# Kernel optimization log

Hardware: AMD Instinct MI355X
Metric: run time of the kernel (lower is better)

Reference implementation:

```python
import jax, jax.numpy as jnp
import numpy as np

CTX = 768   # ctx_len in the original module
C = 768     # n_embd
B = 16
T = 768
K_EPS = 1e-8


def setup_inputs() -> dict:
    key = jax.random.key(0)
    ks = jax.random.split(key, 10)
    scale = 1.0 / np.sqrt(C)
    x = jax.random.normal(ks[0], (B, T, C), jnp.float32)
    time_decay = jax.random.normal(ks[1], (C, 1), jnp.float32) * 0.1
    time_first = jnp.full((C, 1), np.log(0.3), jnp.float32)
    time_mix_k = jax.random.uniform(ks[2], (1, 1, C), jnp.float32)
    time_mix_v = jax.random.uniform(ks[3], (1, 1, C), jnp.float32)
    time_mix_r = jax.random.uniform(ks[4], (1, 1, C), jnp.float32)
    Wk = jax.random.normal(ks[5], (C, C), jnp.float32) * scale
    Wv = jax.random.normal(ks[6], (C, C), jnp.float32) * scale
    Wr = jax.random.normal(ks[7], (C, C), jnp.float32) * scale
    Wo = jax.random.normal(ks[8], (C, C), jnp.float32) * scale
    return {"x": x, "time_decay": time_decay, "time_first": time_first,
            "time_mix_k": time_mix_k, "time_mix_v": time_mix_v, "time_mix_r": time_mix_r,
            "Wk": Wk, "Wv": Wv, "Wr": Wr, "Wo": Wo}


def reference(x, time_decay, time_first, time_mix_k, time_mix_v, time_mix_r, Wk, Wv, Wr, Wo):
    Bb, Tt, Cc = x.shape
    # time_shift: xx[t] = x[t-1], xx[0] = 0
    xx = jnp.pad(x, ((0, 0), (1, 0), (0, 0)))[:, :Tt]
    xk = x * time_mix_k + xx * (1.0 - time_mix_k)
    xv = x * time_mix_v + xx * (1.0 - time_mix_v)
    xr = x * time_mix_r + xx * (1.0 - time_mix_r)
    # projections (nn.Linear, no bias: y = x @ W.T); k, v laid out [B, C, T]
    k = jnp.einsum('btc,oc->bot', xk, Wk)
    v = jnp.einsum('btc,oc->bot', xv, Wv)
    r = jnp.einsum('btc,oc->bto', xr, Wr)
    k = jnp.exp(jnp.minimum(k, 60.0))
    kv = k * v
    # decay kernel: time_w = cat([exp(time_decay)*time_curve, time_first]); w = exp(time_w)[:, -T:]
    curve = (jnp.arange(CTX - 1) - (CTX - 2)).astype(x.dtype)  # [-(CTX-2) .. 0]
    tw = jnp.concatenate([jnp.exp(time_decay) * curve[None, :], time_first], axis=-1)  # [C, CTX]
    w = jnp.exp(tw)[:, -Tt:]            # [C, T]
    kern = w[:, None, :]                # [C, 1, T] depthwise kernel

    def causal_conv(z):  # z: [B, C, T] -> [B, C, T], left-padded cross-correlation
        return jax.lax.conv_general_dilated(
            z, kern, window_strides=(1,), padding=[(Tt - 1, 0)],
            feature_group_count=Cc, dimension_numbers=('NCH', 'OIH', 'NCH'))

    wkv = causal_conv(kv)
    wk = causal_conv(k) + K_EPS
    rwkv = jax.nn.sigmoid(r) * jnp.transpose(wkv / wk, (0, 2, 1))  # [B, T, C]
    return jnp.einsum('btc,oc->bto', rwkv, Wo)
```

## Files before the change

kernel.cpp:

```cpp
#include <hip/hip_runtime.h>
#include <math.h>

#define Mq 12288
#define Nq 768
#define Kq 768
#define Tq 768
#define Bq 16
#define Cq 768
#define BK 64
#define BM 128

typedef __bf16 bf16x8 __attribute__((ext_vector_type(8)));
typedef __bf16 bf16x4 __attribute__((ext_vector_type(4)));
typedef __bf16 bf16x2 __attribute__((ext_vector_type(2)));
typedef float  floatx4 __attribute__((ext_vector_type(4)));

#define GLD_LDS16(g, l) __builtin_amdgcn_global_load_lds(                      \
    (const __attribute__((address_space(1))) unsigned int*)(g),                \
    (__attribute__((address_space(3))) unsigned int*)(l), 16, 0, 0)

__global__ __launch_bounds__(256)
void prep_kernel(const float* __restrict__ x,
                 const float* __restrict__ mk, const float* __restrict__ mv,
                 const float* __restrict__ mr,
                 const float* __restrict__ Wk, const float* __restrict__ Wv,
                 const float* __restrict__ Wr, const float* __restrict__ Wo,
                 __bf16* __restrict__ xk, __bf16* __restrict__ xv,
                 __bf16* __restrict__ xr, __bf16* __restrict__ wp)
{
    const int bid = blockIdx.x;
    if (bid < 9216) {
        const int i  = bid * 256 + threadIdx.x;
        const int c4 = i % (Cq / 4);
        const int m  = i / (Cq / 4);
        const int t  = m % Tq;
        const int c0 = c4 * 4;

        const float4 xc = *(const float4*)(x + (size_t)m * Cq + c0);
        float4 xp = make_float4(0.f, 0.f, 0.f, 0.f);
        if (t > 0) xp = *(const float4*)(x + (size_t)(m - 1) * Cq + c0);

        const float4 k4 = *(const float4*)(mk + c0);
        const float4 v4 = *(const float4*)(mv + c0);
        const float4 r4 = *(const float4*)(mr + c0);

        bf16x4 ok = { (__bf16)fmaf(k4.x, xc.x - xp.x, xp.x),
                      (__bf16)fmaf(k4.y, xc.y - xp.y, xp.y),
                      (__bf16)fmaf(k4.z, xc.z - xp.z, xp.z),
                      (__bf16)fmaf(k4.w, xc.w - xp.w, xp.w) };
        bf16x4 ov = { (__bf16)fmaf(v4.x, xc.x - xp.x, xp.x),
                      (__bf16)fmaf(v4.y, xc.y - xp.y, xp.y),
                      (__bf16)fmaf(v4.z, xc.z - xp.z, xp.z),
                      (__bf16)fmaf(v4.w, xc.w - xp.w, xp.w) };
        bf16x4 orr = { (__bf16)fmaf(r4.x, xc.x - xp.x, xp.x),
                       (__bf16)fmaf(r4.y, xc.y - xp.y, xp.y),
                       (__bf16)fmaf(r4.z, xc.z - xp.z, xp.z),
                       (__bf16)fmaf(r4.w, xc.w - xp.w, xp.w) };
        const size_t o = (size_t)m * Cq + c0;
        *(bf16x4*)(xk + o) = ok;
        *(bf16x4*)(xv + o) = ov;
        *(bf16x4*)(xr + o) = orr;
    } else {
        const int i   = (bid - 9216) * 256 + threadIdx.x;
        const int a   = i / 147456;
        const int off = (i - a * 147456) * 4;
        const float* s = (a == 0) ? Wk : (a == 1) ? Wv : (a == 2) ? Wr : Wo;
        const float4 v = *(const float4*)(s + off);
        bf16x4 r = { (__bf16)v.x, (__bf16)v.y, (__bf16)v.z, (__bf16)v.w };
        *(bf16x4*)(wp + (size_t)a * 589824 + off) = r;
    }
}

template<bool KVR>
__global__ __launch_bounds__(256, 3)
void mfma_gemm(const __bf16* __restrict__ A0, const __bf16* __restrict__ A1,
               const __bf16* __restrict__ A2,
               const __bf16* __restrict__ W,
               __bf16* __restrict__ OUTb, float* __restrict__ OUTf)
{
    __shared__ __bf16 As[BM * BK];
    __shared__ __bf16 Bs[128 * BK];

    const int STRIPS = KVR ? 18 : 6;

    const int i_    = blockIdx.x;
    const int xcd   = i_ & 7;
    const int j_    = i_ >> 3;
    const int strip = j_ % STRIPS;
    const int mt    = xcd * 12 + j_ / STRIPS;

    const int tid   = threadIdx.x;
    const int wave  = tid >> 6;
    const int lane  = tid & 63;
    const int m0    = mt * BM;
    const int matid = KVR ? strip / 6 : 0;
    const int n0    = KVR ? (strip % 6) * 128 : strip * 128;
    const int wn0   = strip * 128;

    const __bf16* A = KVR ? (matid == 0 ? A0 : matid == 1 ? A1 : A2) : A0;

    const int r8 = lane >> 3;
    const int sc = (lane & 7) ^ r8;
    const __bf16* gA[4];  __bf16* lA[4];
    const __bf16* gB[4];  __bf16* lB[4];
#pragma unroll
    for (int i = 0; i < 4; ++i) {
        const int row = (wave * 4 + i) * 8 + r8;
        gA[i] = A + (size_t)(m0 + row) * Kq + sc * 8;
        lA[i] = As + (wave * 4 + i) * 512;
        gB[i] = W + (size_t)(wn0 + row) * Kq + sc * 8;
        lB[i] = Bs + (wave * 4 + i) * 512;
    }

    const int wm   = wave & 1;
    const int wn   = wave >> 1;
    const int xRow = wm * 64 + (lane & 15);
    const int wRow = wn * 64 + (lane & 15);
    const int lk   = lane >> 4;

    floatx4 acc[4][4];
#pragma unroll
    for (int i = 0; i < 4; ++i)
#pragma unroll
        for (int j = 0; j < 4; ++j) acc[i][j] = (floatx4){0.f, 0.f, 0.f, 0.f};

    for (int kt = 0; kt < Kq / BK; ++kt) {
#pragma unroll
        for (int i = 0; i < 4; ++i) { GLD_LDS16(gA[i], lA[i]); gA[i] += BK; }
#pragma unroll
        for (int i = 0; i < 4; ++i) { GLD_LDS16(gB[i], lB[i]); gB[i] += BK; }
        __syncthreads();

#pragma unroll
        for (int kk = 0; kk < 2; ++kk) {
            bf16x8 wF[4], xF[4];
#pragma unroll
            for (int i = 0; i < 4; ++i) {
                const int r = wRow + i * 16;
                wF[i] = *(const bf16x8*)(Bs + r * BK +
                                         (((kk << 2) | lk) ^ (r & 7)) * 8);
            }
#pragma unroll
            for (int j = 0; j < 4; ++j) {
                const int r = xRow + j * 16;
                xF[j] = *(const bf16x8*)(As + r * BK +
                                         (((kk << 2) | lk) ^ (r & 7)) * 8);
            }
#pragma unroll
            for (int i = 0; i < 4; ++i)
#pragma unroll
                for (int j = 0; j < 4; ++j)
                    acc[i][j] = __builtin_amdgcn_mfma_f32_16x16x32_bf16(
                        wF[i], xF[j], acc[i][j], 0, 0, 0);
        }
        __syncthreads();
    }

#pragma unroll
    for (int j = 0; j < 4; ++j) {
        const int tok = m0 + wm * 64 + j * 16 + (lane & 15);
#pragma unroll
        for (int i = 0; i < 4; ++i) {
            const int ch = n0 + wn * 64 + i * 16 + (lane >> 4) * 4;
            if (KVR) {
                float v0 = acc[i][j][0], v1 = acc[i][j][1];
                float v2 = acc[i][j][2], v3 = acc[i][j][3];
                if (matid == 0) {
                    v0 = expf(fminf(v0, 60.f)); v1 = expf(fminf(v1, 60.f));
                    v2 = expf(fminf(v2, 60.f)); v3 = expf(fminf(v3, 60.f));
                } else if (matid == 2) {
                    v0 = 1.f / (1.f + expf(-v0)); v1 = 1.f / (1.f + expf(-v1));
                    v2 = 1.f / (1.f + expf(-v2)); v3 = 1.f / (1.f + expf(-v3));
                }
                bf16x4 o = { (__bf16)v0, (__bf16)v1, (__bf16)v2, (__bf16)v3 };
                *(bf16x4*)(OUTb + (size_t)matid * Mq * Nq +
                           (size_t)tok * Nq + ch) = o;
            } else {
                floatx4 o = acc[i][j];
                *(floatx4*)(OUTf + (size_t)tok * Nq + ch) = o;
            }
        }
    }
}

#define SEG 16
#define SLEN (Tq / SEG)
#define SCH 32

__global__ __launch_bounds__(256)
void scan_kernel(const __bf16* __restrict__ kb, const __bf16* __restrict__ vb,
                 __bf16* rb,
                 const float* __restrict__ td, const float* __restrict__ tf)
{
    __shared__ float2 aS[SEG][SCH / 2];
    __shared__ float2 bS[SEG][SCH / 2];

    const int cx  = threadIdx.x;
    const int seg = threadIdx.y;
    const int c0  = blockIdx.x * SCH + cx * 2;
    const int b   = blockIdx.y;

    const float d0 = expf(td[c0]),     d1 = expf(td[c0 + 1]);
    const float w0 = expf(-d0),        w1 = expf(-d1);
    const float u0 = expf(tf[c0]),     u1 = expf(tf[c0 + 1]);

    const size_t base = ((size_t)b * Tq + seg * SLEN) * Cq + c0;

    float a0 = 0.f, a1 = 0.f, s0 = 0.f, s1 = 0.f;
#pragma unroll 4
    for (int t = 0; t < SLEN; ++t) {
        const size_t idx = base + (size_t)t * Cq;
        const bf16x2 k2 = *(const bf16x2*)(kb + idx);
        const bf16x2 v2 = *(const bf16x2*)(vb + idx);
        const float k0 = (float)k2[0], k1 = (float)k2[1];
        a0 = fmaf(w0, a0, k0 * (float)v2[0]);
        a1 = fmaf(w1, a1, k1 * (float)v2[1]);
        s0 = fmaf(w0, s0, k0);
        s1 = fmaf(w1, s1, k1);
    }
    aS[seg][cx] = make_float2(a0, a1);
    bS[seg][cx] = make_float2(s0, s1);
    __syncthreads();

    if (seg == 0) {
        const float W0 = expf(-d0 * (float)SLEN);
        const float W1 = expf(-d1 * (float)SLEN);
        float ia0 = 0.f, ia1 = 0.f, ib0 = 0.f, ib1 = 0.f;
#pragma unroll
        for (int s = 0; s < SEG; ++s) {
            const float2 ta = aS[s][cx];
            const float2 tb = bS[s][cx];
            aS[s][cx] = make_float2(ia0, ia1);
            bS[s][cx] = make_float2(ib0, ib1);
            ia0 = fmaf(W0, ia0, ta.x);  ia1 = fmaf(W1, ia1, ta.y);
            ib0 = fmaf(W0, ib0, tb.x);  ib1 = fmaf(W1, ib1, tb.y);
        }
    }
    __syncthreads();

    const float2 ain = aS[seg][cx];
    const float2 bin = bS[seg][cx];
    a0 = ain.x; a1 = ain.y; s0 = bin.x; s1 = bin.y;
#pragma unroll 2
    for (int t = 0; t < SLEN; ++t) {
        const size_t idx = base + (size_t)t * Cq;
        const bf16x2 k2 = *(const bf16x2*)(kb + idx);
        const bf16x2 v2 = *(const bf16x2*)(vb + idx);
        const bf16x2 r2 = *(const bf16x2*)(rb + idx);
        const float k0 = (float)k2[0], k1 = (float)k2[1];
        const float kv0 = k0 * (float)v2[0], kv1 = k1 * (float)v2[1];
        const float n0 = fmaf(u0, kv0, a0), n1 = fmaf(u1, kv1, a1);
        const float e0 = fmaf(u0, k0, s0) + 1e-8f;
        const float e1 = fmaf(u1, k1, s1) + 1e-8f;
        bf16x2 o = { (__bf16)((float)r2[0] * n0 / e0),
                     (__bf16)((float)r2[1] * n1 / e1) };
        *(bf16x2*)(rb + idx) = o;
        a0 = fmaf(w0, a0, kv0);  a1 = fmaf(w1, a1, kv1);
        s0 = fmaf(w0, s0, k0);   s1 = fmaf(w1, s1, k1);
    }
}

extern "C" void kernel_launch(void* const* d_in, const int* in_sizes, int n_in,
                              void* d_out, int out_size, void* d_ws, size_t ws_size,
                              hipStream_t stream)
{
    const float* x  = (const float*)d_in[0];
    const float* td = (const float*)d_in[1];
    const float* tf = (const float*)d_in[2];
    const float* mk = (const float*)d_in[3];
    const float* mv = (const float*)d_in[4];
    const float* mr = (const float*)d_in[5];
    const float* Wk = (const float*)d_in[6];
    const float* Wv = (const float*)d_in[7];
    const float* Wr = (const float*)d_in[8];
    const float* Wo = (const float*)d_in[9];

    const size_t MC = (size_t)Mq * Cq;

    __bf16* xk = (__bf16*)d_out;
    __bf16* xv = xk + MC;

    __bf16* xr   = (__bf16*)d_ws;
    __bf16* kbuf = xr + MC;
    __bf16* vbuf = kbuf + MC;
    __bf16* rbuf = vbuf + MC;
    __bf16* Wp   = rbuf + MC;
    __bf16* Wob  = Wp + 3 * 589824;

    prep_kernel<<<11520, 256, 0, stream>>>(x, mk, mv, mr, Wk, Wv, Wr, Wo,
                                           xk, xv, xr, Wp);

    mfma_gemm<true><<<18 * 96, 256, 0, stream>>>(
        xk, xv, xr, Wp, kbuf, nullptr);

    scan_kernel<<<dim3(Cq / SCH, Bq), dim3(SCH / 2, SEG), 0, stream>>>(
        kbuf, vbuf, rbuf, td, tf);

    mfma_gemm<false><<<6 * 96, 256, 0, stream>>>(
        rbuf, nullptr, nullptr, Wob, nullptr, (float*)d_out);
}
```

Measured before the change: 235.1 us.

## Vectorize scan to 8 channels per thread and cache k,v in registers

```diff
diff --git a/kernel.cpp b/kernel.cpp
--- a/kernel.cpp
+++ b/kernel.cpp
@@ -183,80 +183,95 @@
     }
 }
 
-#define SEG 16
-#define SLEN (Tq / SEG)
-#define SCH 32
+#define SSEG 64
+#define SSLEN (Tq / SSEG)
 
 __global__ __launch_bounds__(256)
 void scan_kernel(const __bf16* __restrict__ kb, const __bf16* __restrict__ vb,
                  __bf16* rb,
                  const float* __restrict__ td, const float* __restrict__ tf)
 {
-    __shared__ float2 aS[SEG][SCH / 2];
-    __shared__ float2 bS[SEG][SCH / 2];
-
-    const int cx  = threadIdx.x;
+    __shared__ float aS[SSEG][4][8];
+    __shared__ float bS[SSEG][4][8];
+
+    const int tx  = threadIdx.x;
     const int seg = threadIdx.y;
-    const int c0  = blockIdx.x * SCH + cx * 2;
+    const int c0  = blockIdx.x * 32 + tx * 8;
     const int b   = blockIdx.y;
 
-    const float d0 = expf(td[c0]),     d1 = expf(td[c0 + 1]);
-    const float w0 = expf(-d0),        w1 = expf(-d1);
-    const float u0 = expf(tf[c0]),     u1 = expf(tf[c0 + 1]);
-
-    const size_t base = ((size_t)b * Tq + seg * SLEN) * Cq + c0;
-
-    float a0 = 0.f, a1 = 0.f, s0 = 0.f, s1 = 0.f;
-#pragma unroll 4
-    for (int t = 0; t < SLEN; ++t) {
+    float w[8], u[8], W12[8];
+#pragma unroll
+    for (int j = 0; j < 8; ++j) {
+        const float d = expf(td[c0 + j]);
+        w[j]   = expf(-d);
+        u[j]   = expf(tf[c0 + j]);
+        W12[j] = expf(-d * (float)SSLEN);
+    }
+
+    const size_t base = ((size_t)b * Tq + seg * SSLEN) * Cq + c0;
+
+    bf16x8 kr[SSLEN], vr[SSLEN];
+#pragma unroll
+    for (int t = 0; t < SSLEN; ++t) {
         const size_t idx = base + (size_t)t * Cq;
-        const bf16x2 k2 = *(const bf16x2*)(kb + idx);
-        const bf16x2 v2 = *(const bf16x2*)(vb + idx);
-        const float k0 = (float)k2[0], k1 = (float)k2[1];
-        a0 = fmaf(w0, a0, k0 * (float)v2[0]);
-        a1 = fmaf(w1, a1, k1 * (float)v2[1]);
-        s0 = fmaf(w0, s0, k0);
-        s1 = fmaf(w1, s1, k1);
-    }
-    aS[seg][cx] = make_float2(a0, a1);
-    bS[seg][cx] = make_float2(s0, s1);
+        kr[t] = *(const bf16x8*)(kb + idx);
+        vr[t] = *(const bf16x8*)(vb + idx);
+    }
+
+    float a[8], s[8];
+#pragma unroll
+    for (int j = 0; j < 8; ++j) { a[j] = 0.f; s[j] = 0.f; }
+#pragma unroll
+    for (int t = 0; t < SSLEN; ++t) {
+#pragma unroll
+        for (int j = 0; j < 8; ++j) {
+            const float kf = (float)kr[t][j];
+            const float vf = (float)vr[t][j];
+            a[j] = fmaf(w[j], a[j], kf * vf);
+            s[j] = fmaf(w[j], s[j], kf);
+        }
+    }
+#pragma unroll
+    for (int j = 0; j < 8; ++j) { aS[seg][tx][j] = a[j]; bS[seg][tx][j] = s[j]; }
     __syncthreads();
 
     if (seg == 0) {
-        const float W0 = expf(-d0 * (float)SLEN);
-        const float W1 = expf(-d1 * (float)SLEN);
-        float ia0 = 0.f, ia1 = 0.f, ib0 = 0.f, ib1 = 0.f;
-#pragma unroll
-        for (int s = 0; s < SEG; ++s) {
-            const float2 ta = aS[s][cx];
-            const float2 tb = bS[s][cx];
-            aS[s][cx] = make_float2(ia0, ia1);
-            bS[s][cx] = make_float2(ib0, ib1);
-            ia0 = fmaf(W0, ia0, ta.x);  ia1 = fmaf(W1, ia1, ta.y);
-            ib0 = fmaf(W0, ib0, tb.x);  ib1 = fmaf(W1, ib1, tb.y);
+        float ia[8], ib[8];
+#pragma unroll
+        for (int j = 0; j < 8; ++j) { ia[j] = 0.f; ib[j] = 0.f; }
+        for (int sg = 0; sg < SSEG; ++sg) {
+#pragma unroll
+            for (int j = 0; j < 8; ++j) {
+                const float ta = aS[sg][tx][j];
+                const float tb = bS[sg][tx][j];
+                aS[sg][tx][j] = ia[j];
+                bS[sg][tx][j] = ib[j];
+                ia[j] = fmaf(W12[j], ia[j], ta);
+                ib[j] = fmaf(W12[j], ib[j], tb);
+            }
         }
     }
     __syncthreads();
 
-    const float2 ain = aS[seg][cx];
-    const float2 bin = bS[seg][cx];
-    a0 = ain.x; a1 = ain.y; s0 = bin.x; s1 = bin.y;
-#pragma unroll 2
-    for (int t = 0; t < SLEN; ++t) {
+#pragma unroll
+    for (int j = 0; j < 8; ++j) { a[j] = aS[seg][tx][j]; s[j] = bS[seg][tx][j]; }
+#pragma unroll
+    for (int t = 0; t < SSLEN; ++t) {
         const size_t idx = base + (size_t)t * Cq;
-        const bf16x2 k2 = *(const bf16x2*)(kb + idx);
-        const bf16x2 v2 = *(const bf16x2*)(vb + idx);
-        const bf16x2 r2 = *(const bf16x2*)(rb + idx);
-        const float k0 = (float)k2[0], k1 = (float)k2[1];
-        const float kv0 = k0 * (float)v2[0], kv1 = k1 * (float)v2[1];
-        const float n0 = fmaf(u0, kv0, a0), n1 = fmaf(u1, kv1, a1);
-        const float e0 = fmaf(u0, k0, s0) + 1e-8f;
-        const float e1 = fmaf(u1, k1, s1) + 1e-8f;
-        bf16x2 o = { (__bf16)((float)r2[0] * n0 / e0),
-                     (__bf16)((float)r2[1] * n1 / e1) };
-        *(bf16x2*)(rb + idx) = o;
-        a0 = fmaf(w0, a0, kv0);  a1 = fmaf(w1, a1, kv1);
-        s0 = fmaf(w0, s0, k0);   s1 = fmaf(w1, s1, k1);
+        const bf16x8 r8 = *(const bf16x8*)(rb + idx);
+        bf16x8 o;
+#pragma unroll
+        for (int j = 0; j < 8; ++j) {
+            const float kf = (float)kr[t][j];
+            const float vf = (float)vr[t][j];
+            const float kv = kf * vf;
+            const float num = fmaf(u[j], kv, a[j]);
+            const float den = fmaf(u[j], kf, s[j]) + 1e-8f;
+            o[j] = (__bf16)((float)r8[j] * num / den);
+            a[j] = fmaf(w[j], a[j], kv);
+            s[j] = fmaf(w[j], s[j], kf);
+        }
+        *(bf16x8*)(rb + idx) = o;
     }
 }
 
@@ -293,7 +308,7 @@
     mfma_gemm<true><<<18 * 96, 256, 0, stream>>>(
         xk, xv, xr, Wp, kbuf, nullptr);
 
-    scan_kernel<<<dim3(Cq / SCH, Bq), dim3(SCH / 2, SEG), 0, stream>>>(
+    scan_kernel<<<dim3(Cq / 32, Bq), dim3(4, SSEG), 0, stream>>>(
         kbuf, vbuf, rbuf, td, tf);
 
     mfma_gemm<false><<<6 * 96, 256, 0, stream>>>(
```

Measured after the change: 235.6 us. About the same (+0.2%).
